# Kernel optimization log

Hardware: AMD Instinct MI355X
Metric: run time of the kernel (lower is better)

## Reference

```python
import jax, jax.numpy as jnp
import numpy as np

N_ENT = 1_000_000
N_REL = 1_000
DIM = 128
R_TYPES = 8
E_PER_TYPE = 131_072
SCORE_DIM = 150_000


def setup_inputs() -> dict:
    key = jax.random.key(0)
    k1, k2, k3, k4, k5 = jax.random.split(key, 5)
    ent_table = jax.random.normal(k1, (N_ENT, DIM), dtype=jnp.float32)
    rel_table = jax.random.normal(k2, (N_REL, DIM), dtype=jnp.float32)
    src_idx = jax.random.randint(k3, (R_TYPES, E_PER_TYPE), 0, N_ENT, dtype=jnp.int32)
    dst_idx = jax.random.randint(k4, (R_TYPES, E_PER_TYPE), 0, N_ENT, dtype=jnp.int32)
    rel_idx = jax.random.randint(k5, (R_TYPES, E_PER_TYPE), 0, N_REL, dtype=jnp.int32)
    return {"ent_table": ent_table, "rel_table": rel_table,
            "src_idx": src_idx, "dst_idx": dst_idx, "rel_idx": rel_idx}


def reference(ent_table, rel_table, src_idx, dst_idx, rel_idx):
    # Edge-wise gather: h_emb (src), r_emb (relation), t_emb (dst) -> [R, E, D]
    h = ent_table[src_idx]
    t = ent_table[dst_idx]
    r = rel_table[rel_idx]
    # TransE-style distance score summed over embedding dim: [R, E]
    scores = jnp.sum(h + r - t, axis=-1)
    # Zero-pad each relation type's scores to SCORE_DIM, then concat (flatten)
    pad = SCORE_DIM - scores.shape[1]
    scores = jnp.pad(scores, ((0, 0), (0, pad)))
    return scores.reshape(-1)
```

## Files before the change

### kernel.cpp

```cpp
#include <hip/hip_runtime.h>

#define N_ENT      1000000
#define N_REL      1000
#define DIM        128
#define R_TYPES    8
#define E_PER_TYPE 131072
#define SCORE_DIM  150000

__global__ void row_sum_kernel(const float* __restrict__ table,
                               float* __restrict__ sums,
                               int nrows) {
    const int tid  = blockIdx.x * blockDim.x + threadIdx.x;
    const int lane = tid & 31;
    const int row0 = tid >> 5;
    const int rows_per_pass = (gridDim.x * blockDim.x) >> 5;

    for (int r = row0; r < nrows; r += rows_per_pass) {
        const float4 v =
            reinterpret_cast<const float4*>(table + (size_t)r * DIM)[lane];
        float s = (v.x + v.y) + (v.z + v.w);
#pragma unroll
        for (int off = 16; off > 0; off >>= 1)
            s += __shfl_down(s, off, 32);
        if (lane == 0) sums[r] = s;
    }
}

__global__ void edge_score_kernel(const int* __restrict__ src_idx,
                                  const int* __restrict__ dst_idx,
                                  const int* __restrict__ rel_idx,
                                  const float* __restrict__ ent_sums,
                                  const float* __restrict__ rel_sums,
                                  float* __restrict__ out) {
    const int total = R_TYPES * SCORE_DIM;
    int i = blockIdx.x * blockDim.x + threadIdx.x;
    if (i >= total) return;

    const int rt = i / SCORE_DIM;
    const int e  = i - rt * SCORE_DIM;

    float v = 0.0f;
    if (e < E_PER_TYPE) {
        const int ei = rt * E_PER_TYPE + e;
        const int s  = src_idx[ei];
        const int d  = dst_idx[ei];
        const int rl = rel_idx[ei];
        v = ent_sums[s] + rel_sums[rl] - ent_sums[d];
    }
    out[i] = v;
}

extern "C" void kernel_launch(void* const* d_in, const int* in_sizes, int n_in,
                              void* d_out, int out_size, void* d_ws, size_t ws_size,
                              hipStream_t stream) {
    const float* ent_table = (const float*)d_in[0];
    const float* rel_table = (const float*)d_in[1];
    const int*   src_idx   = (const int*)d_in[2];
    const int*   dst_idx   = (const int*)d_in[3];
    const int*   rel_idx   = (const int*)d_in[4];
    float* out = (float*)d_out;

    float* ent_sums = (float*)d_ws;
    float* rel_sums = (float*)((char*)d_ws + (size_t)N_ENT * sizeof(float));

    row_sum_kernel<<<2048, 256, 0, stream>>>(ent_table, ent_sums, N_ENT);

    {
        const int blocks = (N_REL * 32 + 255) / 256;
        row_sum_kernel<<<blocks, 256, 0, stream>>>(rel_table, rel_sums, N_REL);
    }

    {
        const int total  = R_TYPES * SCORE_DIM;
        const int blocks = (total + 255) / 256;
        edge_score_kernel<<<blocks, 256, 0, stream>>>(
            src_idx, dst_idx, rel_idx, ent_sums, rel_sums, out);
    }
}
```

Measured before the change: 113.7 us.

## Fuse entity and relation row sums, unroll rows, vectorize edge scoring

Merges the entity and relation row-sum launches into a single kernel, so one launch is removed. In that kernel each 32-lane group now handles two rows per iteration to keep more loads in flight. The edge-score kernel now has each thread handle four outputs, using int4 index loads and a float4 store to cut per-element overhead. It relies on SCORE_DIM and E_PER_TYPE being multiples of 4 so that a vector never straddles a type boundary or the padding edge.

```diff
diff --git a/kernel.cpp b/kernel.cpp
--- a/kernel.cpp
+++ b/kernel.cpp
@@ -7,22 +7,46 @@
 #define E_PER_TYPE 131072
 #define SCORE_DIM  150000
 
-__global__ void row_sum_kernel(const float* __restrict__ table,
-                               float* __restrict__ sums,
-                               int nrows) {
-    const int tid  = blockIdx.x * blockDim.x + threadIdx.x;
-    const int lane = tid & 31;
-    const int row0 = tid >> 5;
-    const int rows_per_pass = (gridDim.x * blockDim.x) >> 5;
+__global__ void row_sum_kernel(const float* __restrict__ ent,
+                               const float* __restrict__ rel,
+                               float* __restrict__ ent_sums,
+                               float* __restrict__ rel_sums) {
+    const int tid     = blockIdx.x * blockDim.x + threadIdx.x;
+    const int lane    = tid & 31;
+    const int g       = tid >> 5;
+    const int ngroups = (gridDim.x * blockDim.x) >> 5;
 
-    for (int r = row0; r < nrows; r += rows_per_pass) {
-        const float4 v =
-            reinterpret_cast<const float4*>(table + (size_t)r * DIM)[lane];
-        float s = (v.x + v.y) + (v.z + v.w);
+    for (int r = g; r < N_ENT; r += 2 * ngroups) {
+        const int  r2   = r + ngroups;
+        const bool has2 = (r2 < N_ENT);
+
+        const float4 a =
+            reinterpret_cast<const float4*>(ent + (size_t)r * DIM)[lane];
+        float4 b = make_float4(0.f, 0.f, 0.f, 0.f);
+        if (has2)
+            b = reinterpret_cast<const float4*>(ent + (size_t)r2 * DIM)[lane];
+
+        float s  = (a.x + a.y) + (a.z + a.w);
+        float s2 = (b.x + b.y) + (b.z + b.w);
+#pragma unroll
+        for (int off = 16; off > 0; off >>= 1) {
+            s  += __shfl_down(s,  off, 32);
+            s2 += __shfl_down(s2, off, 32);
+        }
+        if (lane == 0) {
+            ent_sums[r] = s;
+            if (has2) ent_sums[r2] = s2;
+        }
+    }
+
+    if (g < N_REL) {
+        const float4 a =
+            reinterpret_cast<const float4*>(rel + (size_t)g * DIM)[lane];
+        float s = (a.x + a.y) + (a.z + a.w);
 #pragma unroll
         for (int off = 16; off > 0; off >>= 1)
             s += __shfl_down(s, off, 32);
-        if (lane == 0) sums[r] = s;
+        if (lane == 0) rel_sums[g] = s;
     }
 }
 
@@ -32,22 +56,26 @@
                                   const float* __restrict__ ent_sums,
                                   const float* __restrict__ rel_sums,
                                   float* __restrict__ out) {
-    const int total = R_TYPES * SCORE_DIM;
-    int i = blockIdx.x * blockDim.x + threadIdx.x;
-    if (i >= total) return;
+    const int total4 = R_TYPES * SCORE_DIM / 4;
+    const int i = blockIdx.x * blockDim.x + threadIdx.x;
+    if (i >= total4) return;
 
-    const int rt = i / SCORE_DIM;
-    const int e  = i - rt * SCORE_DIM;
+    const int o  = i * 4;
+    const int rt = o / SCORE_DIM;
+    const int e  = o - rt * SCORE_DIM;
 
-    float v = 0.0f;
+    float4 v = make_float4(0.f, 0.f, 0.f, 0.f);
     if (e < E_PER_TYPE) {
         const int ei = rt * E_PER_TYPE + e;
-        const int s  = src_idx[ei];
-        const int d  = dst_idx[ei];
-        const int rl = rel_idx[ei];
-        v = ent_sums[s] + rel_sums[rl] - ent_sums[d];
+        const int4 s4 = *reinterpret_cast<const int4*>(src_idx + ei);
+        const int4 d4 = *reinterpret_cast<const int4*>(dst_idx + ei);
+        const int4 r4 = *reinterpret_cast<const int4*>(rel_idx + ei);
+        v.x = ent_sums[s4.x] + rel_sums[r4.x] - ent_sums[d4.x];
+        v.y = ent_sums[s4.y] + rel_sums[r4.y] - ent_sums[d4.y];
+        v.z = ent_sums[s4.z] + rel_sums[r4.z] - ent_sums[d4.z];
+        v.w = ent_sums[s4.w] + rel_sums[r4.w] - ent_sums[d4.w];
     }
-    out[i] = v;
+    *reinterpret_cast<float4*>(out + o) = v;
 }
 
 extern "C" void kernel_launch(void* const* d_in, const int* in_sizes, int n_in,
@@ -63,16 +91,12 @@
     float* ent_sums = (float*)d_ws;
     float* rel_sums = (float*)((char*)d_ws + (size_t)N_ENT * sizeof(float));
 
-    row_sum_kernel<<<2048, 256, 0, stream>>>(ent_table, ent_sums, N_ENT);
+    row_sum_kernel<<<2048, 256, 0, stream>>>(ent_table, rel_table,
+                                             ent_sums, rel_sums);
 
     {
-        const int blocks = (N_REL * 32 + 255) / 256;
-        row_sum_kernel<<<blocks, 256, 0, stream>>>(rel_table, rel_sums, N_REL);
-    }
-
-    {
-        const int total  = R_TYPES * SCORE_DIM;
-        const int blocks = (total + 255) / 256;
+        const int total4 = R_TYPES * SCORE_DIM / 4;
+        const int blocks = (total4 + 255) / 256;
         edge_score_kernel<<<blocks, 256, 0, stream>>>(
             src_idx, dst_idx, rel_idx, ent_sums, rel_sums, out);
     }
```

Result: slower. 122.7 us (+7.8%).
